# Optimization experiments

Measured on AMD Instinct MI355X. Metric: run time of the kernel, lower is better.

The kernel has to match this reference:

```python
import jax, jax.numpy as jnp
import numpy as np

B, T, I, H, N, M, O = 256, 128, 512, 512, 1024, 512, 512
EPS = 1e-8


def setup_inputs() -> dict:
    key = jax.random.key(0)
    ks = jax.random.split(key, 10)
    rn = lambda k, shape, s: jax.random.normal(k, shape, jnp.float32) * s
    s_h, s_i, s_m = 1.0 / np.sqrt(H), 1.0 / np.sqrt(I), 1.0 / np.sqrt(M)
    return {
        "x": jax.random.normal(ks[0], (B, T, 1, I), jnp.float32),
        "mem0": jnp.full((N, M), 1e-6, jnp.float32),          # memory init fill_(1e-6)
        "wr0": jnp.eye(B, N, dtype=jnp.float32),               # torch.eye(batch, N)
        "ww0": jnp.eye(B, N, dtype=jnp.float32),
        "h0": rn(ks[1], (B, H), 1.0 / H),                      # normal_(0, 1/num_hidden)
        "Wx": rn(ks[2], (I, H), s_i),
        "Wr": rn(ks[3], (M, H), s_m),
        "bh": jnp.zeros((H,), jnp.float32),
        "Whr": rn(ks[4], (H, M + 6), s_h),                      # read head: k,beta,g,s(3),gamma
        "bhr": jnp.zeros((M + 6,), jnp.float32),
        "Whw": rn(ks[5], (H, M + 6), s_h),                      # write head addressing
        "bhw": jnp.zeros((M + 6,), jnp.float32),
        "Wea": rn(ks[6], (H, 2 * M), s_h),                      # write head erase/add
        "bea": jnp.zeros((2 * M,), jnp.float32),
        "Wo": rn(ks[7], (H, O), s_h),
        "bo": jnp.zeros((O,), jnp.float32),
    }


def _address(h, w_prev, mem, Wh, bh_):
    # Standard NTM addressing: content -> interpolate -> shift -> sharpen.
    p = h @ Wh + bh_                                   # (B, M+6)
    k = jnp.tanh(p[:, :M])                             # key (B, M)
    beta = jax.nn.softplus(p[:, M:M + 1])              # strength >= 0
    g = jax.nn.sigmoid(p[:, M + 1:M + 2])              # gate in (0,1)
    s = jax.nn.softmax(p[:, M + 2:M + 5], axis=-1)     # shift over {-1,0,+1}
    gamma = 1.0 + jax.nn.softplus(p[:, M + 5:M + 6])   # sharpen >= 1
    kn = k / (jnp.linalg.norm(k, axis=-1, keepdims=True) + EPS)
    mn = mem / (jnp.linalg.norm(mem, axis=-1, keepdims=True) + EPS)
    wc = jax.nn.softmax(beta * (kn @ mn.T), axis=-1)   # content weights (B, N)
    wg = g * wc + (1.0 - g) * w_prev                   # interpolation (strictly > 0)
    wt = (s[:, 0:1] * jnp.roll(wg, -1, axis=1)
          + s[:, 1:2] * wg
          + s[:, 2:3] * jnp.roll(wg, 1, axis=1))       # circular shift conv
    wp = wt ** gamma
    return wp / (jnp.sum(wp, axis=-1, keepdims=True) + EPS)


def reference(x, mem0, wr0, ww0, h0, Wx, Wr, bh, Whr, bhr, Whw, bhw, Wea, bea, Wo, bo):
    xs = jnp.transpose(x[:, :, 0, :], (1, 0, 2))       # (T, B, I): x.permute(1,0,2,3)

    def step(carry, x_t):
        mem, wr, ww, h = carry
        # write head (get_weights=False): erase/add into memory with prev ww
        ea = h @ Wea + bea
        e = jax.nn.sigmoid(ea[:, :M])                  # (B, M)
        a = jnp.tanh(ea[:, M:])                        # (B, M)
        mem = (mem * (1.0 - jnp.einsum('bn,bm->nm', ww, e) / B)
               + jnp.einsum('bn,bm->nm', ww, a) / B)   # batch-averaged, mem shared (N, M)
        # read head (get_weights=False): r = wr @ M
        r = wr @ mem                                   # (B, M)
        # controller.step(x_t, r)
        h = jnp.tanh(x_t @ Wx + r @ Wr + bh)           # (B, H)
        # new addressing weights from updated hidden + updated memory
        ww = _address(h, ww, mem, Whw, bhw)
        wr = _address(h, wr, mem, Whr, bhr)
        out = jax.nn.sigmoid(h @ Wo + bo)              # (B, O)
        return (mem, wr, ww, h), out

    _, outs = jax.lax.scan(step, (mem0, wr0, ww0, h0), xs)  # outs (T, B, O)
    return jnp.transpose(outs, (1, 0, 2))              # (B, T, O)
```

## Files before the change

kernel.cpp:

```cpp
#include <hip/hip_runtime.h>
#include <math.h>

#define B_ 256
#define T_ 128
#define I_ 512
#define H_ 512
#define N_ 1024
#define M_ 512
#define O_ 512
#define EPS_ 1e-8f
#define NB_ 512

typedef unsigned short u16;
typedef unsigned long long u64;
typedef __attribute__((ext_vector_type(8))) short v8s;
typedef __attribute__((ext_vector_type(4))) float v4f;

#define MFMA(a, b, c) __builtin_amdgcn_mfma_f32_16x16x32_bf16(a, b, c, 0, 0, 0)

#define PL_BIG 1310720
#define PL_WXT 262144
#define PL_WRT 262144
#define PL_MEM 524288
#define PL_W   262144
#define PL_H   131072
#define PL_KH  262144

template <typename T>
__device__ __forceinline__ T lda_(const T* p) {
    return __hip_atomic_load(const_cast<T*>(p), __ATOMIC_RELAXED, __HIP_MEMORY_SCOPE_AGENT);
}
template <typename T>
__device__ __forceinline__ void sta_(T* p, T v) {
    __hip_atomic_store(p, v, __ATOMIC_RELAXED, __HIP_MEMORY_SCOPE_AGENT);
}
__device__ __forceinline__ uint4 ld16_(const u16* p) {
    const u64* q = (const u64*)p;
    u64 lo = __hip_atomic_load(const_cast<u64*>(q), __ATOMIC_RELAXED, __HIP_MEMORY_SCOPE_AGENT);
    u64 hi = __hip_atomic_load(const_cast<u64*>(q + 1), __ATOMIC_RELAXED, __HIP_MEMORY_SCOPE_AGENT);
    uint4 r;
    r.x = (unsigned)lo; r.y = (unsigned)(lo >> 32);
    r.z = (unsigned)hi; r.w = (unsigned)(hi >> 32);
    return r;
}
__device__ __forceinline__ void st64_(u16* p, u16 a, u16 b, u16 c, u16 d) {
    u64 v = (u64)a | ((u64)b << 16) | ((u64)c << 32) | ((u64)d << 48);
    __hip_atomic_store((u64*)p, v, __ATOMIC_RELAXED, __HIP_MEMORY_SCOPE_AGENT);
}

__device__ __forceinline__ float sigm_(float x) { return 1.f / (1.f + expf(-x)); }
__device__ __forceinline__ float softplus_(float x) { return x > 20.f ? x : log1pf(expf(x)); }
__device__ __forceinline__ u16 f2bf(float f) {
    unsigned u = __float_as_uint(f);
    u += 0x7fffu + ((u >> 16) & 1u);
    return (u16)(u >> 16);
}
__device__ __forceinline__ float bf2f(u16 h) { return __uint_as_float((unsigned)h << 16); }
__device__ __forceinline__ void split2(float f, u16& h, u16& m) {
    h = f2bf(f);
    m = f2bf(f - bf2f(h));
}

__device__ __forceinline__ float wave_sum_(float v) {
#pragma unroll
    for (int o = 32; o > 0; o >>= 1) v += __shfl_down(v, o);
    return v;
}
__device__ __forceinline__ float wave_max_(float v) {
#pragma unroll
    for (int o = 32; o > 0; o >>= 1) v = fmaxf(v, __shfl_down(v, o));
    return v;
}
__device__ float block_sum_(float v, float* s) {
    int lane = threadIdx.x & 63, wid = threadIdx.x >> 6, nw = blockDim.x >> 6;
    v = wave_sum_(v);
    if (lane == 0) s[wid] = v;
    __syncthreads();
    float r = (threadIdx.x < nw) ? s[threadIdx.x] : 0.f;
    if (wid == 0) { r = wave_sum_(r); if (lane == 0) s[0] = r; }
    __syncthreads();
    float out = s[0];
    __syncthreads();
    return out;
}
__device__ float block_max_(float v, float* s) {
    int lane = threadIdx.x & 63, wid = threadIdx.x >> 6, nw = blockDim.x >> 6;
    v = wave_max_(v);
    if (lane == 0) s[wid] = v;
    __syncthreads();
    float r = (threadIdx.x < nw) ? s[threadIdx.x] : -3.4e38f;
    if (wid == 0) { r = wave_max_(r); if (lane == 0) s[0] = r; }
    __syncthreads();
    float out = s[0];
    __syncthreads();
    return out;
}

__device__ __forceinline__ void gsync(unsigned* slots, unsigned* flag, unsigned epoch) {
    __syncthreads();
    if (threadIdx.x == 0)
        __hip_atomic_store(&slots[blockIdx.x * 16], epoch, __ATOMIC_RELAXED,
                           __HIP_MEMORY_SCOPE_AGENT);
    if (blockIdx.x == 0) {
        while (__hip_atomic_load(&slots[threadIdx.x * 16], __ATOMIC_RELAXED,
                                 __HIP_MEMORY_SCOPE_AGENT) < epoch)
            __builtin_amdgcn_s_sleep(1);
        while (__hip_atomic_load(&slots[(threadIdx.x + 256) * 16], __ATOMIC_RELAXED,
                                 __HIP_MEMORY_SCOPE_AGENT) < epoch)
            __builtin_amdgcn_s_sleep(1);
        __syncthreads();
        if (threadIdx.x == 0)
            __hip_atomic_store(flag, epoch, __ATOMIC_RELAXED, __HIP_MEMORY_SCOPE_AGENT);
    } else if (threadIdx.x == 0) {
        while (__hip_atomic_load(flag, __ATOMIC_RELAXED, __HIP_MEMORY_SCOPE_AGENT) < epoch)
            __builtin_amdgcn_s_sleep(1);
    }
    __syncthreads();
}

struct EpiEA0 {
    const float* bea; u16* eT; u16* aT;
    __device__ void operator()(int r0, int c, v4f v) const {
#pragma unroll
        for (int r = 0; r < 4; r++) {
            float val = v[r] + bea[c];
            u16* dst;
            int b = r0 + r;
            if (c < M_) { val = sigm_(val); dst = eT + (size_t)c * B_ + b; }
            else        { val = tanhf(val); dst = aT + (size_t)(c - M_) * B_ + b; }
            u16 h, m; split2(val, h, m);
            dst[0] = h; dst[PL_H] = m;
        }
    }
};
struct EpiR {
    u16* rp;
    __device__ void operator()(int r0, int c, v4f v) const {
#pragma unroll
        for (int r = 0; r < 4; r++) {
            u16 h, m; split2(v[r], h, m);
            size_t idx = (size_t)(r0 + r) * M_ + c;
            sta_(rp + idx, h); sta_(rp + PL_H + idx, m);
        }
    }
};
struct EpiH {
    const float* xwxt; const float* bh; float* hf; u16* hp;
    __device__ void operator()(int r0, int c, v4f v) const {
#pragma unroll
        for (int r = 0; r < 4; r++) {
            int b = r0 + r;
            float val = tanhf(v[r] + xwxt[(size_t)b * (T_ * O_) + c] + bh[c]);
            size_t idx = (size_t)b * H_ + c;
            sta_(hf + idx, val);
            u16 h, m; split2(val, h, m);
            sta_(hp + idx, h); sta_(hp + PL_H + idx, m);
        }
    }
};
struct EpiFused {
    const float* bhw; const float* bhr; const float* bo; const float* bea;
    u16* khp; float* outt; u16* eT; u16* aT;
    __device__ void operator()(int r0, int c, v4f v) const {
        if (c < 1024) {
            int head = c >> 9, key = c & 511;
            const float* bb = head ? bhr : bhw;
#pragma unroll
            for (int r = 0; r < 4; r++) {
                float val = tanhf(v[r] + bb[key]);
                size_t idx = (size_t)(head * 256 + r0 + r) * M_ + key;
                u16 h, m; split2(val, h, m);
                sta_(khp + idx, h); sta_(khp + PL_KH + idx, m);
            }
        } else if (c < 1536) {
            int o = c - 1024;
#pragma unroll
            for (int r = 0; r < 4; r++)
                outt[(size_t)(r0 + r) * (T_ * O_) + o] = sigm_(v[r] + bo[o]);
        } else {
            int m = c - 1536;
#pragma unroll
            for (int r = 0; r < 4; r++) {
                float val = v[r] + bea[m];
                u16* dst;
                int b = r0 + r;
                if (m < M_) { val = sigm_(val); dst = eT + (size_t)m * B_ + b; }
                else        { val = tanhf(val); dst = aT + (size_t)(m - M_) * B_ + b; }
                u16 h, mm; split2(val, h, mm);
                sta_(dst, h); sta_(dst + PL_H, mm);
            }
        }
    }
};

struct NtmArgs {
    const u16 *BigT, *WxT, *WrT;
    u16 *mem_pl, *memT_pl, *wwT_pl, *wr_pl, *h_pl, *r_pl, *eT_pl, *aT_pl, *kh_pl;
    float *memf, *wwf, *wrf, *hf, *logits, *ssqp;
    const float *w6w, *w6r, *bh, *bhw, *bhr, *bea, *bo;
    float* out;
    unsigned* slots;
    unsigned* flag;
};

template <bool AS, bool BS, class Epi>
__device__ __forceinline__ void dev_gemm32(char* smc, const u16* __restrict__ Ap, int lda, int apl,
                                           const u16* __restrict__ Bp, int ldb, int bpl,
                                           int K, int row0, int col0, const Epi& epi) {
    typedef u16 (*AsT)[32][40];
    typedef u16 (*BsT)[64][40];
    AsT As = (AsT)smc;
    BsT Bs = (BsT)(smc + 5120);
    const int tid = threadIdx.x, lane = tid & 63, w = tid >> 6;
    const int wy = w >> 1, wx = w & 1, q = lane >> 4, l15 = lane & 15;
    uint4 ra, rb[2];
    auto loadA = [&](int k0) {
        int s = tid, p = s >> 7, rr = (s >> 2) & 31, kg = s & 3;
        const u16* ap = Ap + (size_t)p * apl + (size_t)(row0 + rr) * lda + k0 + kg * 8;
        ra = AS ? ld16_(ap) : *(const uint4*)ap;
    };
    auto loadB = [&](int k0) {
#pragma unroll
        for (int j = 0; j < 2; j++) {
            int s = j * 256 + tid, p = s >> 8, rr = (s >> 2) & 63, kg = s & 3;
            const u16* bp = Bp + (size_t)p * bpl + (size_t)(col0 + rr) * ldb + k0 + kg * 8;
            rb[j] = BS ? ld16_(bp) : *(const uint4*)bp;
        }
    };
    v4f acc[2] = {};
    loadA(0); loadB(0);
    for (int k0 = 0; k0 < K; k0 += 32) {
        {
            int s = tid, p = s >> 7, rr = (s >> 2) & 31, kg = s & 3;
            *(uint4*)&As[p][rr][kg * 8] = ra;
        }
#pragma unroll
        for (int j = 0; j < 2; j++) {
            int s = j * 256 + tid, p = s >> 8, rr = (s >> 2) & 63, kg = s & 3;
            *(uint4*)&Bs[p][rr][kg * 8] = rb[j];
        }
        __syncthreads();
        if (k0 + 32 < K) { loadA(k0 + 32); loadB(k0 + 32); }
        v8s af0 = *(const v8s*)&As[0][wy * 16 + l15][q * 8];
        v8s af1 = *(const v8s*)&As[1][wy * 16 + l15][q * 8];
        v8s bf[2][2];
#pragma unroll
        for (int nt = 0; nt < 2; nt++) {
            bf[nt][0] = *(const v8s*)&Bs[0][wx * 32 + nt * 16 + l15][q * 8];
            bf[nt][1] = *(const v8s*)&Bs[1][wx * 32 + nt * 16 + l15][q * 8];
        }
#pragma unroll
        for (int nt = 0; nt < 2; nt++) {
            v4f c = acc[nt];
            c = MFMA(af0, bf[nt][0], c);
            c = MFMA(af0, bf[nt][1], c);
            c = MFMA(af1, bf[nt][0], c);
            acc[nt] = c;
        }
        __syncthreads();
    }
#pragma unroll
    for (int nt = 0; nt < 2; nt++)
        epi(row0 + wy * 16 + q * 4, col0 + wx * 32 + nt * 16 + l15, acc[nt]);
}

template <bool AS, bool BS, class Epi>
__device__ __forceinline__ void dev_gemm64(char* smc, const u16* __restrict__ Ap, int lda, int apl,
                                           const u16* __restrict__ Bp, int ldb, int bpl,
                                           int K, int row0, int col0, const Epi& epi) {
    typedef u16 (*T64)[64][40];
    T64 As = (T64)smc;
    T64 Bs = (T64)(smc + 10240);
    const int tid = threadIdx.x, lane = tid & 63, w = tid >> 6;
    const int wy = w >> 1, wx = w & 1, q = lane >> 4, l15 = lane & 15;
    uint4 ra[2], rb[2];
    auto loadAll = [&](int k0) {
#pragma unroll
        for (int j = 0; j < 2; j++) {
            int s = j * 256 + tid, p = s >> 8, rr = (s >> 2) & 63, kg = s & 3;
            const u16* ap = Ap + (size_t)p * apl + (size_t)(row0 + rr) * lda + k0 + kg * 8;
            const u16* bp = Bp + (size_t)p * bpl + (size_t)(col0 + rr) * ldb + k0 + kg * 8;
            ra[j] = AS ? ld16_(ap) : *(const uint4*)ap;
            rb[j] = BS ? ld16_(bp) : *(const uint4*)bp;
        }
    };
    v4f acc[2][2] = {};
    loadAll(0);
    for (int k0 = 0; k0 < K; k0 += 32) {
#pragma unroll
        for (int j = 0; j < 2; j++) {
            int s = j * 256 + tid, p = s >> 8, rr = (s >> 2) & 63, kg = s & 3;
            *(uint4*)&As[p][rr][kg * 8] = ra[j];
            *(uint4*)&Bs[p][rr][kg * 8] = rb[j];
        }
        __syncthreads();
        if (k0 + 32 < K) loadAll(k0 + 32);
        v8s af[2][2], bf[2][2];
#pragma unroll
        for (int mt = 0; mt < 2; mt++) {
            af[mt][0] = *(const v8s*)&As[0][wy * 32 + mt * 16 + l15][q * 8];
            af[mt][1] = *(const v8s*)&As[1][wy * 32 + mt * 16 + l15][q * 8];
            bf[mt][0] = *(const v8s*)&Bs[0][wx * 32 + mt * 16 + l15][q * 8];
            bf[mt][1] = *(const v8s*)&Bs[1][wx * 32 + mt * 16 + l15][q * 8];
        }
#pragma unroll
        for (int mt = 0; mt < 2; mt++)
#pragma unroll
            for (int nt = 0; nt < 2; nt++) {
                v4f c = acc[mt][nt];
                c = MFMA(af[mt][0], bf[nt][0], c);
                c = MFMA(af[mt][0], bf[nt][1], c);
                c = MFMA(af[mt][1], bf[nt][0], c);
                acc[mt][nt] = c;
            }
        __syncthreads();
    }
#pragma unroll
    for (int mt = 0; mt < 2; mt++)
#pragma unroll
        for (int nt = 0; nt < 2; nt++)
            epi(row0 + wy * 32 + mt * 16 + q * 4, col0 + wx * 32 + nt * 16 + l15, acc[mt][nt]);
}

__device__ void dev_memupd(char* smc, int bid, const NtmArgs& A) {
    typedef u16 (*T64)[64][40];
    T64 As = (T64)smc;
    T64 Be = (T64)(smc + 10240);
    T64 Ba = (T64)(smc + 20480);
    float* ssqs = (float*)(smc + 30720);
    const int tid = threadIdx.x, lane = tid & 63, w = tid >> 6;
    const int wy = w >> 1, wx = w & 1, q = lane >> 4, l15 = lane & 15;
    const int bx = bid & 7, by = bid >> 3;
    const int row0 = by * 64, col0 = bx * 64;
    if (tid < 64) ssqs[tid] = 0.f;
    uint4 rA[2], rE[2], rB[2];
    auto loadAll = [&](int k0) {
#pragma unroll
        for (int j = 0; j < 2; j++) {
            int s = j * 256 + tid, p = s >> 8, rr = (s >> 2) & 63, kg = s & 3;
            rA[j] = ld16_(A.wwT_pl + (size_t)p * PL_W + (size_t)(row0 + rr) * B_ + k0 + kg * 8);
            rE[j] = ld16_(A.eT_pl + (size_t)p * PL_H + (size_t)(col0 + rr) * B_ + k0 + kg * 8);
            rB[j] = ld16_(A.aT_pl + (size_t)p * PL_H + (size_t)(col0 + rr) * B_ + k0 + kg * 8);
        }
    };
    v4f ae[2][2] = {}, aa[2][2] = {};
    loadAll(0);
    for (int k0 = 0; k0 < B_; k0 += 32) {
#pragma unroll
        for (int j = 0; j < 2; j++) {
            int s = j * 256 + tid, p = s >> 8, rr = (s >> 2) & 63, kg = s & 3;
            *(uint4*)&As[p][rr][kg * 8] = rA[j];
            *(uint4*)&Be[p][rr][kg * 8] = rE[j];
            *(uint4*)&Ba[p][rr][kg * 8] = rB[j];
        }
        __syncthreads();
        if (k0 + 32 < B_) loadAll(k0 + 32);
        v8s af[2][2], be[2][2], ba[2][2];
#pragma unroll
        for (int mt = 0; mt < 2; mt++) {
            af[mt][0] = *(const v8s*)&As[0][wy * 32 + mt * 16 + l15][q * 8];
            af[mt][1] = *(const v8s*)&As[1][wy * 32 + mt * 16 + l15][q * 8];
            be[mt][0] = *(const v8s*)&Be[0][wx * 32 + mt * 16 + l15][q * 8];
            be[mt][1] = *(const v8s*)&Be[1][wx * 32 + mt * 16 + l15][q * 8];
            ba[mt][0] = *(const v8s*)&Ba[0][wx * 32 + mt * 16 + l15][q * 8];
            ba[mt][1] = *(const v8s*)&Ba[1][wx * 32 + mt * 16 + l15][q * 8];
        }
#pragma unroll
        for (int mt = 0; mt < 2; mt++)
#pragma unroll
            for (int nt = 0; nt < 2; nt++) {
                v4f c = ae[mt][nt];
                c = MFMA(af[mt][0], be[nt][0], c);
                c = MFMA(af[mt][0], be[nt][1], c);
                c = MFMA(af[mt][1], be[nt][0], c);
                ae[mt][nt] = c;
                v4f d = aa[mt][nt];
                d = MFMA(af[mt][0], ba[nt][0], d);
                d = MFMA(af[mt][0], ba[nt][1], d);
                d = MFMA(af[mt][1], ba[nt][0], d);
                aa[mt][nt] = d;
            }
        __syncthreads();
    }
    const float invB = 1.f / (float)B_;
#pragma unroll
    for (int mt = 0; mt < 2; mt++)
#pragma unroll
        for (int nt = 0; nt < 2; nt++) {
            int r0 = row0 + wy * 32 + mt * 16 + q * 4;
            int c  = col0 + wx * 32 + nt * 16 + l15;
            u16 hv[4][2];
#pragma unroll
            for (int r = 0; r < 4; r++) {
                size_t idx = (size_t)(r0 + r) * M_ + c;
                float old = A.memf[idx];
                float nv = old * (1.f - ae[mt][nt][r] * invB) + aa[mt][nt][r] * invB;
                A.memf[idx] = nv;
                u16 h, m; split2(nv, h, m);
                sta_(A.mem_pl + idx, h); sta_(A.mem_pl + PL_MEM + idx, m);
                hv[r][0] = h; hv[r][1] = m;
                atomicAdd(&ssqs[r0 + r - row0], nv * nv);
            }
            size_t tb = (size_t)c * N_ + r0;
            st64_(A.memT_pl + tb, hv[0][0], hv[1][0], hv[2][0], hv[3][0]);
            st64_(A.memT_pl + PL_MEM + tb, hv[0][1], hv[1][1], hv[2][1], hv[3][1]);
        }
    __syncthreads();
    if (tid < 64) sta_(A.ssqp + (size_t)(row0 + tid) * 8 + bx, ssqs[tid]);
}

__device__ void dev_logits(char* smc, int bx, int by, const NtmArgs& A) {
    typedef u16 (*T64)[64][40];
    T64 As = (T64)smc;
    T64 Bs = (T64)(smc + 10240);
    float* invn_s = (float*)(smc + 20480);
    const int tid = threadIdx.x, lane = tid & 63, w = tid >> 6;
    const int wy = w >> 1, wx = w & 1, q = lane >> 4, l15 = lane & 15;
    const int row0 = by * 64, col0 = bx * 64;
    if (tid < 64) {
        float s = 0.f;
#pragma unroll
        for (int j = 0; j < 8; j++) s += lda_(A.ssqp + (size_t)(col0 + tid) * 8 + j);
        invn_s[tid] = 1.f / (sqrtf(s) + EPS_);
    }
    uint4 ra[2], rb[2];
    auto loadAll = [&](int k0) {
#pragma unroll
        for (int j = 0; j < 2; j++) {
            int s = j * 256 + tid, p = s >> 8, rr = (s >> 2) & 63, kg = s & 3;
            ra[j] = ld16_(A.kh_pl + (size_t)p * PL_KH + (size_t)(row0 + rr) * M_ + k0 + kg * 8);
            rb[j] = ld16_(A.mem_pl + (size_t)p * PL_MEM + (size_t)(col0 + rr) * M_ + k0 + kg * 8);
        }
    };
    v4f acc[2][2] = {};
    loadAll(0);
    for (int k0 = 0; k0 < M_; k0 += 32) {
#pragma unroll
        for (int j = 0; j < 2; j++) {
            int s = j * 256 + tid, p = s >> 8, rr = (s >> 2) & 63, kg = s & 3;
            *(uint4*)&As[p][rr][kg * 8] = ra[j];
            *(uint4*)&Bs[p][rr][kg * 8] = rb[j];
        }
        __syncthreads();
        if (k0 + 32 < M_) loadAll(k0 + 32);
        v8s af[2][2], bf[2][2];
#pragma unroll
        for (int mt = 0; mt < 2; mt++) {
            af[mt][0] = *(const v8s*)&As[0][wy * 32 + mt * 16 + l15][q * 8];
            af[mt][1] = *(const v8s*)&As[1][wy * 32 + mt * 16 + l15][q * 8];
            bf[mt][0] = *(const v8s*)&Bs[0][wx * 32 + mt * 16 + l15][q * 8];
            bf[mt][1] = *(const v8s*)&Bs[1][wx * 32 + mt * 16 + l15][q * 8];
        }
#pragma unroll
        for (int mt = 0; mt < 2; mt++)
#pragma unroll
            for (int nt = 0; nt < 2; nt++) {
                v4f c = acc[mt][nt];
                c = MFMA(af[mt][0], bf[nt][0], c);
                c = MFMA(af[mt][0], bf[nt][1], c);
                c = MFMA(af[mt][1], bf[nt][0], c);
                acc[mt][nt] = c;
            }
        __syncthreads();
    }
#pragma unroll
    for (int mt = 0; mt < 2; mt++)
#pragma unroll
        for (int nt = 0; nt < 2; nt++) {
            int r0 = row0 + wy * 32 + mt * 16 + q * 4;
            int c  = col0 + wx * 32 + nt * 16 + l15;
            float in_ = invn_s[c - col0];
#pragma unroll
            for (int r = 0; r < 4; r++)
                sta_(A.logits + (size_t)(r0 + r) * N_ + c, acc[mt][nt][r] * in_);
        }
}

__device__ void dev_addr(char* smc, int row, const NtmArgs& A) {
    float* wgs = (float*)smc;
    float* red = (float*)(smc + 4096);
    int head = row >> 8, b = row & 255;
    const float* w6 = head ? A.w6r : A.w6w;
    const float* bias = head ? A.bhr : A.bhw;
    float* wf = head ? A.wrf : A.wwf;
    int tid = threadIdx.x;
    float d0 = 0, d1 = 0, d2 = 0, d3 = 0, d4 = 0, d5 = 0, ssq = 0;
#pragma unroll
    for (int j = 0; j < 2; j++) {
        int k = tid + j * 256;
        float hv = lda_(A.hf + (size_t)b * H_ + k);
        const float* wk = w6 + k * 6;
        d0 += hv * wk[0]; d1 += hv * wk[1]; d2 += hv * wk[2];
        d3 += hv * wk[3]; d4 += hv * wk[4]; d5 += hv * wk[5];
        size_t ki = (size_t)row * M_ + k;
        float kv = bf2f(lda_(A.kh_pl + ki)) + bf2f(lda_(A.kh_pl + PL_KH + ki));
        ssq += kv * kv;
    }
    d0 = block_sum_(d0, red); d1 = block_sum_(d1, red); d2 = block_sum_(d2, red);
    d3 = block_sum_(d3, red); d4 = block_sum_(d4, red); d5 = block_sum_(d5, red);
    ssq = block_sum_(ssq, red);
    float beta = softplus_(d0 + bias[M_]);
    float g = sigm_(d1 + bias[M_ + 1]);
    float a0 = d2 + bias[M_ + 2], a1 = d3 + bias[M_ + 3], a2 = d4 + bias[M_ + 4];
    float mx3 = fmaxf(a0, fmaxf(a1, a2));
    float e0 = expf(a0 - mx3), e1 = expf(a1 - mx3), e2 = expf(a2 - mx3);
    float es = e0 + e1 + e2;
    float s0 = e0 / es, s1 = e1 / es, s2 = e2 / es;
    float gamma = 1.f + softplus_(d5 + bias[M_ + 5]);
    float rowsc = beta / (sqrtf(ssq) + EPS_);
    const u64* lp = (const u64*)(A.logits + (size_t)row * N_ + tid * 4);
    u64 la = lda_(lp), lb = lda_(lp + 1);
    float l[4];
    l[0] = __uint_as_float((unsigned)la) * rowsc;
    l[1] = __uint_as_float((unsigned)(la >> 32)) * rowsc;
    l[2] = __uint_as_float((unsigned)lb) * rowsc;
    l[3] = __uint_as_float((unsigned)(lb >> 32)) * rowsc;
    float mx = fmaxf(fmaxf(l[0], l[1]), fmaxf(l[2], l[3]));
    mx = block_max_(mx, red);
    float ex[4], sum = 0.f;
#pragma unroll
    for (int j = 0; j < 4; j++) { ex[j] = expf(l[j] - mx); sum += ex[j]; }
    sum = block_sum_(sum, red);
    float inv = 1.f / sum;
    float wprev[4];
#pragma unroll
    for (int j = 0; j < 4; j++) wprev[j] = wf[(size_t)b * N_ + tid * 4 + j];
#pragma unroll
    for (int j = 0; j < 4; j++) wgs[tid * 4 + j] = g * ex[j] * inv + (1.f - g) * wprev[j];
    __syncthreads();
    float wp[4], psum = 0.f;
#pragma unroll
    for (int j = 0; j < 4; j++) {
        int n = tid * 4 + j;
        float wt = s0 * wgs[(n + 1) & (N_ - 1)] + s1 * wgs[n] + s2 * wgs[(n - 1) & (N_ - 1)];
        float v = expf(gamma * logf(wt));
        wp[j] = v; psum += v;
    }
    psum = block_sum_(psum, red);
    float invp = 1.f / (psum + EPS_);
#pragma unroll
    for (int j = 0; j < 4; j++) {
        int n = tid * 4 + j;
        float val = wp[j] * invp;
        wf[(size_t)b * N_ + n] = val;
        u16 h, m; split2(val, h, m);
        if (head == 0) {
            size_t tb = (size_t)n * B_ + b;
            sta_(A.wwT_pl + tb, h); sta_(A.wwT_pl + PL_W + tb, m);
        } else {
            size_t idx = (size_t)b * N_ + n;
            sta_(A.wr_pl + idx, h); sta_(A.wr_pl + PL_W + idx, m);
        }
    }
}

__global__ __launch_bounds__(256, 2) void ntm_loop(NtmArgs A) {
    __shared__ __align__(16) char sm[31232];
    const int bid = blockIdx.x;
    unsigned ep = 0;
    for (int t = 0; t < T_; t++) {
        if (bid < 128) dev_memupd(sm, bid, A);
        gsync(A.slots, A.flag, ++ep);
        if (bid < 32) {
            int bx = bid & 7, by = bid >> 3;
            dev_gemm64<true, true>(sm, A.wr_pl, 1024, PL_W, A.memT_pl, 1024, PL_MEM, 1024,
                                   by * 64, bx * 64, EpiR{A.r_pl});
        }
        gsync(A.slots, A.flag, ++ep);
        if (bid < 32) {
            int bx = bid & 7, by = bid >> 3;
            dev_gemm64<true, false>(sm, A.r_pl, 512, PL_H, A.WrT, 512, PL_WRT, 512,
                                    by * 64, bx * 64,
                                    EpiH{A.out + (size_t)t * O_, A.bh, A.hf, A.h_pl});
        }
        gsync(A.slots, A.flag, ++ep);
        if (bid < 320) {
            int g = bid & 7, idx = bid >> 3;
            int bx = g * 5 + idx % 5, by = idx / 5;
            dev_gemm32<true, false>(sm, A.h_pl, 512, PL_H, A.BigT, 512, PL_BIG, 512,
                                    by * 32, bx * 64,
                                    EpiFused{A.bhw, A.bhr, A.bo, A.bea, A.kh_pl,
                                             A.out + (size_t)t * O_, A.eT_pl, A.aT_pl});
        }
        gsync(A.slots, A.flag, ++ep);
        if (bid < 128) {
            int g = bid & 7, idx = bid >> 3;
            int bx = g * 2 + (idx & 1), by = idx >> 1;
            dev_logits(sm, bx, by, A);
        }
        gsync(A.slots, A.flag, ++ep);
        for (int row = bid; row < 2 * B_; row += NB_) dev_addr(sm, row, A);
        gsync(A.slots, A.flag, ++ep);
    }
}

template <int TM, class Epi>
__global__ __launch_bounds__(256) void gemm2(const u16* __restrict__ Ap, int lda, int apl,
                                             const u16* __restrict__ Bp, int ldb, int bpl,
                                             int K, Epi epi) {
    constexpr int AL = (TM * 32 * 2) / (256 * 8);
    constexpr int MT = TM / 32;
    __shared__ u16 As[2][TM][40];
    __shared__ u16 Bs[2][64][40];
    const int tid = threadIdx.x, lane = tid & 63, w = tid >> 6;
    const int wy = w >> 1, wx = w & 1, q = lane >> 4, l15 = lane & 15;
    const int row0 = blockIdx.y * TM, col0 = blockIdx.x * 64;
    uint4 ra[AL], rb[2];
    auto loadA = [&](int k0) {
#pragma unroll
        for (int j = 0; j < AL; j++) {
            int s = j * 256 + tid, p = s / (TM * 4), rr = (s >> 2) % TM, kg = s & 3;
            ra[j] = *(const uint4*)(Ap + (size_t)p * apl + (size_t)(row0 + rr) * lda + k0 + kg * 8);
        }
    };
    auto loadB = [&](int k0) {
#pragma unroll
        for (int j = 0; j < 2; j++) {
            int s = j * 256 + tid, p = s >> 8, rr = (s >> 2) & 63, kg = s & 3;
            rb[j] = *(const uint4*)(Bp + (size_t)p * bpl + (size_t)(col0 + rr) * ldb + k0 + kg * 8);
        }
    };
    v4f acc[MT][2] = {};
    loadA(0); loadB(0);
    for (int k0 = 0; k0 < K; k0 += 32) {
#pragma unroll
        for (int j = 0; j < AL; j++) {
            int s = j * 256 + tid, p = s / (TM * 4), rr = (s >> 2) % TM, kg = s & 3;
            *(uint4*)&As[p][rr][kg * 8] = ra[j];
        }
#pragma unroll
        for (int j = 0; j < 2; j++) {
            int s = j * 256 + tid, p = s >> 8, rr = (s >> 2) & 63, kg = s & 3;
            *(uint4*)&Bs[p][rr][kg * 8] = rb[j];
        }
        __syncthreads();
        if (k0 + 32 < K) { loadA(k0 + 32); loadB(k0 + 32); }
        v8s af[MT][2], bf[2][2];
#pragma unroll
        for (int mt = 0; mt < MT; mt++) {
            af[mt][0] = *(const v8s*)&As[0][wy * (TM / 2) + mt * 16 + l15][q * 8];
            af[mt][1] = *(const v8s*)&As[1][wy * (TM / 2) + mt * 16 + l15][q * 8];
        }
#pragma unroll
        for (int nt = 0; nt < 2; nt++) {
            bf[nt][0] = *(const v8s*)&Bs[0][wx * 32 + nt * 16 + l15][q * 8];
            bf[nt][1] = *(const v8s*)&Bs[1][wx * 32 + nt * 16 + l15][q * 8];
        }
#pragma unroll
        for (int mt = 0; mt < MT; mt++)
#pragma unroll
            for (int nt = 0; nt < 2; nt++) {
                v4f c = acc[mt][nt];
                c = MFMA(af[mt][0], bf[nt][0], c);
                c = MFMA(af[mt][0], bf[nt][1], c);
                c = MFMA(af[mt][1], bf[nt][0], c);
                acc[mt][nt] = c;
            }
        __syncthreads();
    }
#pragma unroll
    for (int mt = 0; mt < MT; mt++)
#pragma unroll
        for (int nt = 0; nt < 2; nt++)
            epi(row0 + wy * (TM / 2) + mt * 16 + q * 4, col0 + wx * 32 + nt * 16 + l15, acc[mt][nt]);
}

__global__ __launch_bounds__(256) void gemm2_xwx(const float* __restrict__ x, const u16* __restrict__ WxT,
                                                 float* __restrict__ outbuf) {
    __shared__ u16 As[2][64][40];
    __shared__ u16 Bs[2][64][40];
    const int tid = threadIdx.x, lane = tid & 63, w = tid >> 6;
    const int wy = w >> 1, wx = w & 1, q = lane >> 4, l15 = lane & 15;
    const int row0 = blockIdx.y * 64, col0 = blockIdx.x * 64;
    const int sr = tid >> 2, ss = (tid & 3) * 8;
    const int arow = row0 + sr, ab = arow & 255, at = arow >> 8;
    const float* Asrc = x + ((size_t)ab * T_ + at) * I_ + ss;
    v4f acc[2][2] = {};
    for (int k0 = 0; k0 < I_; k0 += 32) {
        float4 f0 = *(const float4*)(Asrc + k0);
        float4 f1 = *(const float4*)(Asrc + k0 + 4);
        float av8[8] = {f0.x, f0.y, f0.z, f0.w, f1.x, f1.y, f1.z, f1.w};
#pragma unroll
        for (int j = 0; j < 8; j++) {
            u16 h, m; split2(av8[j], h, m);
            As[0][sr][ss + j] = h; As[1][sr][ss + j] = m;
        }
#pragma unroll
        for (int p = 0; p < 2; p++)
            *(uint4*)&Bs[p][sr][ss] = *(const uint4*)&WxT[(size_t)p * PL_WXT + (size_t)(col0 + sr) * I_ + k0 + ss];
        __syncthreads();
        v8s af[2][2], bf[2][2];
#pragma unroll
        for (int mt = 0; mt < 2; mt++) {
            af[mt][0] = *(const v8s*)&As[0][wy * 32 + mt * 16 + l15][q * 8];
            af[mt][1] = *(const v8s*)&As[1][wy * 32 + mt * 16 + l15][q * 8];
            bf[mt][0] = *(const v8s*)&Bs[0][wx * 32 + mt * 16 + l15][q * 8];
            bf[mt][1] = *(const v8s*)&Bs[1][wx * 32 + mt * 16 + l15][q * 8];
        }
#pragma unroll
        for (int mt = 0; mt < 2; mt++)
#pragma unroll
            for (int nt = 0; nt < 2; nt++) {
                v4f c = acc[mt][nt];
                c = MFMA(af[mt][0], bf[nt][0], c);
                c = MFMA(af[mt][0], bf[nt][1], c);
                c = MFMA(af[mt][1], bf[nt][0], c);
                acc[mt][nt] = c;
            }
        __syncthreads();
    }
#pragma unroll
    for (int mt = 0; mt < 2; mt++)
#pragma unroll
        for (int nt = 0; nt < 2; nt++) {
            int r0 = row0 + wy * 32 + mt * 16 + q * 4;
            int c  = col0 + wx * 32 + nt * 16 + l15;
#pragma unroll
            for (int r = 0; r < 4; r++) {
                int row = r0 + r, b = row & 255, t = row >> 8;
                outbuf[((size_t)b * T_ + t) * O_ + c] = acc[mt][nt][r];
            }
        }
}

__global__ __launch_bounds__(256) void decomp_t(const float* __restrict__ in, int ldin, int c0,
                                                int R, u16* __restrict__ outp, int opl) {
    __shared__ float Ls[32][33];
    const int r0 = blockIdx.x * 32, cB = blockIdx.y * 32;
    const int tid = threadIdx.x;
    int lr = tid >> 3, lc = (tid & 7) * 4;
#pragma unroll
    for (int j = 0; j < 4; j++)
        Ls[lr][lc + j] = in[(size_t)(r0 + lr) * ldin + c0 + cB + lc + j];
    __syncthreads();
    int lc2 = tid >> 3, lr2 = (tid & 7) * 4;
    u16 hv[4], mv[4];
#pragma unroll
    for (int j = 0; j < 4; j++) split2(Ls[lr2 + j][lc2], hv[j], mv[j]);
    size_t base = (size_t)(cB + lc2) * R + r0 + lr2;
    *(ushort4*)&outp[0 * (size_t)opl + base] = make_ushort4(hv[0], hv[1], hv[2], hv[3]);
    *(ushort4*)&outp[1 * (size_t)opl + base] = make_ushort4(mv[0], mv[1], mv[2], mv[3]);
}

__global__ __launch_bounds__(512) void wh6_kernel(const float* __restrict__ Whw, const float* __restrict__ Whr,
                                                  float* __restrict__ w6w, float* __restrict__ w6r,
                                                  unsigned* __restrict__ barz) {
    int k = threadIdx.x;
    if (blockIdx.x == 0) {
        for (int i = k; i < NB_ * 16 + 16; i += 512) barz[i] = 0u;
    }
    const float* src = blockIdx.x ? Whr : Whw;
    float* dst = blockIdx.x ? w6r : w6w;
#pragma unroll
    for (int j = 0; j < 6; j++) dst[k * 6 + j] = src[(size_t)k * (M_ + 6) + M_ + j];
}
__global__ __launch_bounds__(256) void init_mem(const float* __restrict__ mem0, float* __restrict__ memf,
                                                u16* __restrict__ mem_pl, u16* __restrict__ memT_pl) {
    int n = blockIdx.x;
    for (int c = threadIdx.x; c < M_; c += 256) {
        float v = mem0[(size_t)n * M_ + c];
        size_t idx = (size_t)n * M_ + c;
        memf[idx] = v;
        u16 h, m; split2(v, h, m);
        mem_pl[idx] = h; mem_pl[PL_MEM + idx] = m;
        size_t tb = (size_t)c * N_ + n;
        memT_pl[tb] = h; memT_pl[PL_MEM + tb] = m;
    }
}
__global__ __launch_bounds__(256) void init_w(const float* __restrict__ wr0, const float* __restrict__ ww0,
                                              float* __restrict__ wrf, float* __restrict__ wwf,
                                              u16* __restrict__ wr_pl, u16* __restrict__ wwT_pl) {
    int b = blockIdx.x;
    for (int n = threadIdx.x; n < N_; n += 256) {
        size_t idx = (size_t)b * N_ + n;
        float vw = ww0[idx]; wwf[idx] = vw;
        u16 h, m; split2(vw, h, m);
        size_t tb = (size_t)n * B_ + b;
        wwT_pl[tb] = h; wwT_pl[PL_W + tb] = m;
        float vr = wr0[idx]; wrf[idx] = vr;
        split2(vr, h, m);
        wr_pl[idx] = h; wr_pl[PL_W + idx] = m;
    }
}
__global__ __launch_bounds__(64) void init_h(const float* __restrict__ h0, float* __restrict__ hf,
                                             u16* __restrict__ hp) {
    int b = blockIdx.x;
    for (int c = threadIdx.x; c < H_; c += 64) {
        size_t idx = (size_t)b * H_ + c;
        float v = h0[idx];
        hf[idx] = v;
        u16 h, m; split2(v, h, m);
        hp[idx] = h; hp[PL_H + idx] = m;
    }
}

extern "C" void kernel_launch(void* const* d_in, const int* in_sizes, int n_in,
                              void* d_out, int out_size, void* d_ws, size_t ws_size,
                              hipStream_t stream) {
    (void)in_sizes; (void)n_in; (void)out_size; (void)ws_size;
    const float* x    = (const float*)d_in[0];
    const float* mem0 = (const float*)d_in[1];
    const float* wr0  = (const float*)d_in[2];
    const float* ww0  = (const float*)d_in[3];
    const float* h0   = (const float*)d_in[4];
    const float* Wx   = (const float*)d_in[5];
    const float* Wr   = (const float*)d_in[6];
    const float* bh   = (const float*)d_in[7];
    const float* Whr  = (const float*)d_in[8];
    const float* bhr  = (const float*)d_in[9];
    const float* Whw  = (const float*)d_in[10];
    const float* bhw  = (const float*)d_in[11];
    const float* Wea  = (const float*)d_in[12];
    const float* bea  = (const float*)d_in[13];
    const float* Wo   = (const float*)d_in[14];
    const float* bo   = (const float*)d_in[15];
    float* out = (float*)d_out;

    char* wsb = (char*)d_ws;
    size_t off = 0;
    auto carveU = [&](size_t elems) { u16* p = (u16*)(wsb + off); off += elems * sizeof(u16); return p; };
    u16* BigT    = carveU(2 * (size_t)PL_BIG);
    u16* WxT     = carveU(2 * (size_t)PL_WXT);
    u16* WrT     = carveU(2 * (size_t)PL_WRT);
    u16* mem_pl  = carveU(2 * (size_t)PL_MEM);
    u16* memT_pl = carveU(2 * (size_t)PL_MEM);
    u16* wwT_pl  = carveU(2 * (size_t)PL_W);
    u16* wr_pl   = carveU(2 * (size_t)PL_W);
    u16* h_pl    = carveU(2 * (size_t)PL_H);
    u16* r_pl    = carveU(2 * (size_t)PL_H);
    u16* eT_pl   = carveU(2 * (size_t)PL_H);
    u16* aT_pl   = carveU(2 * (size_t)PL_H);
    u16* kh_pl   = carveU(2 * (size_t)PL_KH);
    auto carveF = [&](size_t elems) { float* p = (float*)(wsb + off); off += elems * sizeof(float); return p; };
    float* memf   = carveF((size_t)N_ * M_);
    float* wwf    = carveF((size_t)B_ * N_);
    float* wrf    = carveF((size_t)B_ * N_);
    float* hf     = carveF((size_t)B_ * H_);
    float* logits = carveF((size_t)2 * B_ * N_);
    float* ssqp   = carveF((size_t)N_ * 8);
    float* w6w    = carveF(H_ * 6);
    float* w6r    = carveF(H_ * 6);
    off = (off + 127) & ~(size_t)127;
    unsigned* slots = (unsigned*)(wsb + off);
    unsigned* flag  = slots + NB_ * 16;
    off += (NB_ * 16 + 16) * sizeof(unsigned) + 64;

    decomp_t<<<dim3(16, 16), 256, 0, stream>>>(Whw, M_ + 6, 0, 512, BigT, PL_BIG);
    decomp_t<<<dim3(16, 16), 256, 0, stream>>>(Whr, M_ + 6, 0, 512, BigT + (size_t)512 * 512, PL_BIG);
    decomp_t<<<dim3(16, 16), 256, 0, stream>>>(Wo, 512, 0, 512, BigT + (size_t)1024 * 512, PL_BIG);
    decomp_t<<<dim3(16, 32), 256, 0, stream>>>(Wea, 1024, 0, 512, BigT + (size_t)1536 * 512, PL_BIG);
    decomp_t<<<dim3(16, 16), 256, 0, stream>>>(Wx, 512, 0, 512, WxT, PL_WXT);
    decomp_t<<<dim3(16, 16), 256, 0, stream>>>(Wr, 512, 0, 512, WrT, PL_WRT);
    wh6_kernel<<<2, 512, 0, stream>>>(Whw, Whr, w6w, w6r, slots);
    init_mem<<<N_, 256, 0, stream>>>(mem0, memf, mem_pl, memT_pl);
    init_w<<<B_, 256, 0, stream>>>(wr0, ww0, wrf, wwf, wr_pl, wwT_pl);
    init_h<<<B_, 64, 0, stream>>>(h0, hf, h_pl);
    gemm2_xwx<<<dim3(8, 512), 256, 0, stream>>>(x, WxT, out);
    gemm2<32, EpiEA0><<<dim3(16, 8), 256, 0, stream>>>(
        h_pl, 512, PL_H, BigT + (size_t)1536 * 512, 512, PL_BIG, 512, EpiEA0{bea, eT_pl, aT_pl});

    NtmArgs A;
    A.BigT = BigT; A.WxT = WxT; A.WrT = WrT;
    A.mem_pl = mem_pl; A.memT_pl = memT_pl; A.wwT_pl = wwT_pl; A.wr_pl = wr_pl;
    A.h_pl = h_pl; A.r_pl = r_pl; A.eT_pl = eT_pl; A.aT_pl = aT_pl; A.kh_pl = kh_pl;
    A.memf = memf; A.wwf = wwf; A.wrf = wrf; A.hf = hf; A.logits = logits; A.ssqp = ssqp;
    A.w6w = w6w; A.w6r = w6r; A.bh = bh; A.bhw = bhw; A.bhr = bhr; A.bea = bea; A.bo = bo;
    A.out = out;
    A.slots = slots;
    A.flag = flag;
    ntm_loop<<<dim3(NB_), dim3(256), 0, stream>>>(A);
}
```

Before: 17.16 ms.

## Widen GEMM K-tiles to 64 and overlap fused head GEMM with logits

```diff
diff --git a/kernel.cpp b/kernel.cpp
--- a/kernel.cpp
+++ b/kernel.cpp
@@ -204,122 +204,144 @@
 };
 
 template <bool AS, bool BS, class Epi>
-__device__ __forceinline__ void dev_gemm32(char* smc, const u16* __restrict__ Ap, int lda, int apl,
-                                           const u16* __restrict__ Bp, int ldb, int bpl,
-                                           int K, int row0, int col0, const Epi& epi) {
-    typedef u16 (*AsT)[32][40];
-    typedef u16 (*BsT)[64][40];
-    AsT As = (AsT)smc;
-    BsT Bs = (BsT)(smc + 5120);
+__device__ __forceinline__ void dev_g64(char* smc, const u16* __restrict__ Ap, int lda, int apl,
+                                        const u16* __restrict__ Bp, int ldb, int bpl,
+                                        int K, int row0, int col0, const Epi& epi) {
+    typedef u16 (*T72)[64][72];
+    T72 As = (T72)smc;
+    T72 Bs = (T72)(smc + 18432);
     const int tid = threadIdx.x, lane = tid & 63, w = tid >> 6;
     const int wy = w >> 1, wx = w & 1, q = lane >> 4, l15 = lane & 15;
-    uint4 ra, rb[2];
+    uint4 ra[4], rb[4];
     auto loadA = [&](int k0) {
-        int s = tid, p = s >> 7, rr = (s >> 2) & 31, kg = s & 3;
-        const u16* ap = Ap + (size_t)p * apl + (size_t)(row0 + rr) * lda + k0 + kg * 8;
-        ra = AS ? ld16_(ap) : *(const uint4*)ap;
+#pragma unroll
+        for (int j = 0; j < 4; j++) {
+            int s = j * 256 + tid, p = s >> 9, rr = (s >> 3) & 63, kg = s & 7;
+            const u16* ap = Ap + (size_t)p * apl + (size_t)(row0 + rr) * lda + k0 + kg * 8;
+            ra[j] = AS ? ld16_(ap) : *(const uint4*)ap;
+        }
     };
     auto loadB = [&](int k0) {
 #pragma unroll
-        for (int j = 0; j < 2; j++) {
-            int s = j * 256 + tid, p = s >> 8, rr = (s >> 2) & 63, kg = s & 3;
+        for (int j = 0; j < 4; j++) {
+            int s = j * 256 + tid, p = s >> 9, rr = (s >> 3) & 63, kg = s & 7;
             const u16* bp = Bp + (size_t)p * bpl + (size_t)(col0 + rr) * ldb + k0 + kg * 8;
             rb[j] = BS ? ld16_(bp) : *(const uint4*)bp;
         }
     };
-    v4f acc[2] = {};
+    v4f acc[2][2] = {};
     loadA(0); loadB(0);
-    for (int k0 = 0; k0 < K; k0 += 32) {
-        {
-            int s = tid, p = s >> 7, rr = (s >> 2) & 31, kg = s & 3;
-            *(uint4*)&As[p][rr][kg * 8] = ra;
-        }
-#pragma unroll
-        for (int j = 0; j < 2; j++) {
-            int s = j * 256 + tid, p = s >> 8, rr = (s >> 2) & 63, kg = s & 3;
+    for (int k0 = 0; k0 < K; k0 += 64) {
+#pragma unroll
+        for (int j = 0; j < 4; j++) {
+            int s = j * 256 + tid, p = s >> 9, rr = (s >> 3) & 63, kg = s & 7;
+            *(uint4*)&As[p][rr][kg * 8] = ra[j];
             *(uint4*)&Bs[p][rr][kg * 8] = rb[j];
         }
         __syncthreads();
-        if (k0 + 32 < K) { loadA(k0 + 32); loadB(k0 + 32); }
-        v8s af0 = *(const v8s*)&As[0][wy * 16 + l15][q * 8];
-        v8s af1 = *(const v8s*)&As[1][wy * 16 + l15][q * 8];
-        v8s bf[2][2];
-#pragma unroll
-        for (int nt = 0; nt < 2; nt++) {
-            bf[nt][0] = *(const v8s*)&Bs[0][wx * 32 + nt * 16 + l15][q * 8];
-            bf[nt][1] = *(const v8s*)&Bs[1][wx * 32 + nt * 16 + l15][q * 8];
-        }
-#pragma unroll
-        for (int nt = 0; nt < 2; nt++) {
-            v4f c = acc[nt];
-            c = MFMA(af0, bf[nt][0], c);
-            c = MFMA(af0, bf[nt][1], c);
-            c = MFMA(af1, bf[nt][0], c);
-            acc[nt] = c;
-        }
-        __syncthreads();
-    }
-#pragma unroll
-    for (int nt = 0; nt < 2; nt++)
-        epi(row0 + wy * 16 + q * 4, col0 + wx * 32 + nt * 16 + l15, acc[nt]);
-}
-
-template <bool AS, bool BS, class Epi>
-__device__ __forceinline__ void dev_gemm64(char* smc, const u16* __restrict__ Ap, int lda, int apl,
-                                           const u16* __restrict__ Bp, int ldb, int bpl,
-                                           int K, int row0, int col0, const Epi& epi) {
-    typedef u16 (*T64)[64][40];
-    T64 As = (T64)smc;
-    T64 Bs = (T64)(smc + 10240);
+        if (k0 + 64 < K) { loadA(k0 + 64); loadB(k0 + 64); }
+        v8s af[2][2][2], bf[2][2][2];
+#pragma unroll
+        for (int mt = 0; mt < 2; mt++)
+#pragma unroll
+            for (int p = 0; p < 2; p++)
+#pragma unroll
+                for (int h = 0; h < 2; h++) {
+                    af[mt][p][h] = *(const v8s*)&As[p][wy * 32 + mt * 16 + l15][h * 32 + q * 8];
+                    bf[mt][p][h] = *(const v8s*)&Bs[p][wx * 32 + mt * 16 + l15][h * 32 + q * 8];
+                }
+#pragma unroll
+        for (int mt = 0; mt < 2; mt++)
+#pragma unroll
+            for (int nt = 0; nt < 2; nt++) {
+                v4f c = acc[mt][nt];
+#pragma unroll
+                for (int h = 0; h < 2; h++) {
+                    c = MFMA(af[mt][0][h], bf[nt][0][h], c);
+                    c = MFMA(af[mt][0][h], bf[nt][1][h], c);
+                    c = MFMA(af[mt][1][h], bf[nt][0][h], c);
+                }
+                acc[mt][nt] = c;
+            }
+        __syncthreads();
+    }
+#pragma unroll
+    for (int mt = 0; mt < 2; mt++)
+#pragma unroll
+        for (int nt = 0; nt < 2; nt++)
+            epi(row0 + wy * 32 + mt * 16 + q * 4, col0 + wx * 32 + nt * 16 + l15, acc[mt][nt]);
+}
+
+template <class Epi>
+__device__ __forceinline__ void dev_g32x128(char* smc, const u16* __restrict__ Ap, int lda, int apl,
+                                            const u16* __restrict__ Bp, int ldb, int bpl,
+                                            int K, int row0, int col0, const Epi& epi) {
+    typedef u16 (*TA)[32][72];
+    typedef u16 (*TB)[128][72];
+    TA As = (TA)smc;
+    TB Bs = (TB)(smc + 9216);
     const int tid = threadIdx.x, lane = tid & 63, w = tid >> 6;
     const int wy = w >> 1, wx = w & 1, q = lane >> 4, l15 = lane & 15;
-    uint4 ra[2], rb[2];
-    auto loadAll = [&](int k0) {
+    uint4 ra[2], rb[8];
+    auto loadA = [&](int k0) {
 #pragma unroll
         for (int j = 0; j < 2; j++) {
-            int s = j * 256 + tid, p = s >> 8, rr = (s >> 2) & 63, kg = s & 3;
-            const u16* ap = Ap + (size_t)p * apl + (size_t)(row0 + rr) * lda + k0 + kg * 8;
-            const u16* bp = Bp + (size_t)p * bpl + (size_t)(col0 + rr) * ldb + k0 + kg * 8;
-            ra[j] = AS ? ld16_(ap) : *(const uint4*)ap;
-            rb[j] = BS ? ld16_(bp) : *(const uint4*)bp;
+            int s = j * 256 + tid, p = s >> 8, rr = (s >> 3) & 31, kg = s & 7;
+            ra[j] = ld16_(Ap + (size_t)p * apl + (size_t)(row0 + rr) * lda + k0 + kg * 8);
         }
     };
-    v4f acc[2][2] = {};
-    loadAll(0);
-    for (int k0 = 0; k0 < K; k0 += 32) {
+    auto loadB = [&](int k0) {
+#pragma unroll
+        for (int j = 0; j < 8; j++) {
+            int s = j * 256 + tid, p = s >> 10, rr = (s >> 3) & 127, kg = s & 7;
+            rb[j] = *(const uint4*)(Bp + (size_t)p * bpl + (size_t)(col0 + rr) * ldb + k0 + kg * 8);
+        }
+    };
+    v4f acc[4] = {};
+    loadA(0); loadB(0);
+    for (int k0 = 0; k0 < K; k0 += 64) {
 #pragma unroll
         for (int j = 0; j < 2; j++) {
-            int s = j * 256 + tid, p = s >> 8, rr = (s >> 2) & 63, kg = s & 3;
+            int s = j * 256 + tid, p = s >> 8, rr = (s >> 3) & 31, kg = s & 7;
             *(uint4*)&As[p][rr][kg * 8] = ra[j];
+        }
+#pragma unroll
+        for (int j = 0; j < 8; j++) {
+            int s = j * 256 + tid, p = s >> 10, rr = (s >> 3) & 127, kg = s & 7;
             *(uint4*)&Bs[p][rr][kg * 8] = rb[j];
         }
         __syncthreads();
-        if (k0 + 32 < K) loadAll(k0 + 32);
-        v8s af[2][2], bf[2][2];
-#pragma unroll
-        for (int mt = 0; mt < 2; mt++) {
-            af[mt][0] = *(const v8s*)&As[0][wy * 32 + mt * 16 + l15][q * 8];
-            af[mt][1] = *(const v8s*)&As[1][wy * 32 + mt * 16 + l15][q * 8];
-            bf[mt][0] = *(const v8s*)&Bs[0][wx * 32 + mt * 16 + l15][q * 8];
-            bf[mt][1] = *(const v8s*)&Bs[1][wx * 32 + mt * 16 + l15][q * 8];
-        }
-#pragma unroll
-        for (int mt = 0; mt < 2; mt++)
-#pragma unroll
-            for (int nt = 0; nt < 2; nt++) {
-                v4f c = acc[mt][nt];
-                c = MFMA(af[mt][0], bf[nt][0], c);
-                c = MFMA(af[mt][0], bf[nt][1], c);
-                c = MFMA(af[mt][1], bf[nt][0], c);
-                acc[mt][nt] = c;
+        if (k0 + 64 < K) { loadA(k0 + 64); loadB(k0 + 64); }
+        v8s af[2][2];
+#pragma unroll
+        for (int p = 0; p < 2; p++)
+#pragma unroll
+            for (int h = 0; h < 2; h++)
+                af[p][h] = *(const v8s*)&As[p][wy * 16 + l15][h * 32 + q * 8];
+        v8s bf[4][2][2];
+#pragma unroll
+        for (int nt = 0; nt < 4; nt++)
+#pragma unroll
+            for (int p = 0; p < 2; p++)
+#pragma unroll
+                for (int h = 0; h < 2; h++)
+                    bf[nt][p][h] = *(const v8s*)&Bs[p][wx * 64 + nt * 16 + l15][h * 32 + q * 8];
+#pragma unroll
+        for (int nt = 0; nt < 4; nt++) {
+            v4f c = acc[nt];
+#pragma unroll
+            for (int h = 0; h < 2; h++) {
+                c = MFMA(af[0][h], bf[nt][0][h], c);
+                c = MFMA(af[0][h], bf[nt][1][h], c);
+                c = MFMA(af[1][h], bf[nt][0][h], c);
             }
-        __syncthreads();
-    }
-#pragma unroll
-    for (int mt = 0; mt < 2; mt++)
-#pragma unroll
-        for (int nt = 0; nt < 2; nt++)
-            epi(row0 + wy * 32 + mt * 16 + q * 4, col0 + wx * 32 + nt * 16 + l15, acc[mt][nt]);
+            acc[nt] = c;
+        }
+        __syncthreads();
+    }
+#pragma unroll
+    for (int nt = 0; nt < 4; nt++)
+        epi(row0 + wy * 16 + q * 4, col0 + wx * 64 + nt * 16 + l15, acc[nt]);
 }
 
 __device__ void dev_memupd(char* smc, int bid, const NtmArgs& A) {
@@ -410,10 +432,10 @@
 }
 
 __device__ void dev_logits(char* smc, int bx, int by, const NtmArgs& A) {
-    typedef u16 (*T64)[64][40];
-    T64 As = (T64)smc;
-    T64 Bs = (T64)(smc + 10240);
-    float* invn_s = (float*)(smc + 20480);
+    typedef u16 (*T72)[64][72];
+    T72 As = (T72)smc;
+    T72 Bs = (T72)(smc + 18432);
+    float* invn_s = (float*)(smc + 36864);
     const int tid = threadIdx.x, lane = tid & 63, w = tid >> 6;
     const int wy = w >> 1, wx = w & 1, q = lane >> 4, l15 = lane & 15;
     const int row0 = by * 64, col0 = bx * 64;
@@ -423,42 +445,47 @@
         for (int j = 0; j < 8; j++) s += lda_(A.ssqp + (size_t)(col0 + tid) * 8 + j);
         invn_s[tid] = 1.f / (sqrtf(s) + EPS_);
     }
-    uint4 ra[2], rb[2];
+    uint4 ra[4], rb[4];
     auto loadAll = [&](int k0) {
 #pragma unroll
-        for (int j = 0; j < 2; j++) {
-            int s = j * 256 + tid, p = s >> 8, rr = (s >> 2) & 63, kg = s & 3;
+        for (int j = 0; j < 4; j++) {
+            int s = j * 256 + tid, p = s >> 9, rr = (s >> 3) & 63, kg = s & 7;
             ra[j] = ld16_(A.kh_pl + (size_t)p * PL_KH + (size_t)(row0 + rr) * M_ + k0 + kg * 8);
             rb[j] = ld16_(A.mem_pl + (size_t)p * PL_MEM + (size_t)(col0 + rr) * M_ + k0 + kg * 8);
         }
     };
     v4f acc[2][2] = {};
     loadAll(0);
-    for (int k0 = 0; k0 < M_; k0 += 32) {
-#pragma unroll
-        for (int j = 0; j < 2; j++) {
-            int s = j * 256 + tid, p = s >> 8, rr = (s >> 2) & 63, kg = s & 3;
+    for (int k0 = 0; k0 < M_; k0 += 64) {
+#pragma unroll
+        for (int j = 0; j < 4; j++) {
+            int s = j * 256 + tid, p = s >> 9, rr = (s >> 3) & 63, kg = s & 7;
             *(uint4*)&As[p][rr][kg * 8] = ra[j];
             *(uint4*)&Bs[p][rr][kg * 8] = rb[j];
         }
         __syncthreads();
-        if (k0 + 32 < M_) loadAll(k0 + 32);
-        v8s af[2][2], bf[2][2];
-#pragma unroll
-        for (int mt = 0; mt < 2; mt++) {
-            af[mt][0] = *(const v8s*)&As[0][wy * 32 + mt * 16 + l15][q * 8];
-            af[mt][1] = *(const v8s*)&As[1][wy * 32 + mt * 16 + l15][q * 8];
-            bf[mt][0] = *(const v8s*)&Bs[0][wx * 32 + mt * 16 + l15][q * 8];
-            bf[mt][1] = *(const v8s*)&Bs[1][wx * 32 + mt * 16 + l15][q * 8];
-        }
+        if (k0 + 64 < M_) loadAll(k0 + 64);
+        v8s af[2][2][2], bf[2][2][2];
+#pragma unroll
+        for (int mt = 0; mt < 2; mt++)
+#pragma unroll
+            for (int p = 0; p < 2; p++)
+#pragma unroll
+                for (int h = 0; h < 2; h++) {
+                    af[mt][p][h] = *(const v8s*)&As[p][wy * 32 + mt * 16 + l15][h * 32 + q * 8];
+                    bf[mt][p][h] = *(const v8s*)&Bs[p][wx * 32 + mt * 16 + l15][h * 32 + q * 8];
+                }
 #pragma unroll
         for (int mt = 0; mt < 2; mt++)
 #pragma unroll
             for (int nt = 0; nt < 2; nt++) {
                 v4f c = acc[mt][nt];
-                c = MFMA(af[mt][0], bf[nt][0], c);
-                c = MFMA(af[mt][0], bf[nt][1], c);
-                c = MFMA(af[mt][1], bf[nt][0], c);
+#pragma unroll
+                for (int h = 0; h < 2; h++) {
+                    c = MFMA(af[mt][0][h], bf[nt][0][h], c);
+                    c = MFMA(af[mt][0][h], bf[nt][1][h], c);
+                    c = MFMA(af[mt][1][h], bf[nt][0][h], c);
+                }
                 acc[mt][nt] = c;
             }
         __syncthreads();
@@ -555,7 +582,7 @@
 }
 
 __global__ __launch_bounds__(256, 2) void ntm_loop(NtmArgs A) {
-    __shared__ __align__(16) char sm[31232];
+    __shared__ __align__(16) char sm[47104];
     const int bid = blockIdx.x;
     unsigned ep = 0;
     for (int t = 0; t < T_; t++) {
@@ -563,30 +590,36 @@
         gsync(A.slots, A.flag, ++ep);
         if (bid < 32) {
             int bx = bid & 7, by = bid >> 3;
-            dev_gemm64<true, true>(sm, A.wr_pl, 1024, PL_W, A.memT_pl, 1024, PL_MEM, 1024,
-                                   by * 64, bx * 64, EpiR{A.r_pl});
+            dev_g64<true, true>(sm, A.wr_pl, 1024, PL_W, A.memT_pl, 1024, PL_MEM, 1024,
+                                by * 64, bx * 64, EpiR{A.r_pl});
         }
         gsync(A.slots, A.flag, ++ep);
         if (bid < 32) {
             int bx = bid & 7, by = bid >> 3;
-            dev_gemm64<true, false>(sm, A.r_pl, 512, PL_H, A.WrT, 512, PL_WRT, 512,
-                                    by * 64, bx * 64,
-                                    EpiH{A.out + (size_t)t * O_, A.bh, A.hf, A.h_pl});
+            dev_g64<true, false>(sm, A.r_pl, 512, PL_H, A.WrT, 512, PL_WRT, 512,
+                                 by * 64, bx * 64,
+                                 EpiH{A.out + (size_t)t * O_, A.bh, A.hf, A.h_pl});
         }
         gsync(A.slots, A.flag, ++ep);
-        if (bid < 320) {
-            int g = bid & 7, idx = bid >> 3;
-            int bx = g * 5 + idx % 5, by = idx / 5;
-            dev_gemm32<true, false>(sm, A.h_pl, 512, PL_H, A.BigT, 512, PL_BIG, 512,
-                                    by * 32, bx * 64,
-                                    EpiFused{A.bhw, A.bhr, A.bo, A.bea, A.kh_pl,
-                                             A.out + (size_t)t * O_, A.eT_pl, A.aT_pl});
+        if (bid < 64) {
+            int bx = bid & 7, by = bid >> 3;
+            dev_g32x128(sm, A.h_pl, 512, PL_H, A.BigT, 512, PL_BIG, 512,
+                        by * 32, bx * 128,
+                        EpiFused{A.bhw, A.bhr, A.bo, A.bea, A.kh_pl,
+                                 A.out + (size_t)t * O_, A.eT_pl, A.aT_pl});
         }
         gsync(A.slots, A.flag, ++ep);
         if (bid < 128) {
             int g = bid & 7, idx = bid >> 3;
             int bx = g * 2 + (idx & 1), by = idx >> 1;
             dev_logits(sm, bx, by, A);
+        } else if (bid < 224) {
+            int b2 = bid - 128;
+            int bx = 8 + b2 % 12, by = b2 / 12;
+            dev_g32x128(sm, A.h_pl, 512, PL_H, A.BigT, 512, PL_BIG, 512,
+                        by * 32, bx * 128,
+                        EpiFused{A.bhw, A.bhr, A.bo, A.bea, A.kh_pl,
+                                 A.out + (size_t)t * O_, A.eT_pl, A.aT_pl});
         }
         gsync(A.slots, A.flag, ++ep);
         for (int row = bid; row < 2 * B_; row += NB_) dev_addr(sm, row, A);
```

Result: slower. 26.08 ms (+52.0%).
